# Kernel tuning notes

Hardware: AMD Instinct MI355X
Metric: run time of the kernel (lower is better)

## Reference

```python
import jax, jax.numpy as jnp
import numpy as np

N_HEAD, D_HEAD, D_MODEL = 8, 64, 512
QLEN, MLEN, BSZ = 1024, 1024, 4
KLEN = QLEN + MLEN
SCALE = 1.0 / (D_HEAD ** 0.5)
LN_EPS = 1e-5


def _rel_shift(x):
    # x: [qlen, rlen, bsz, n_head]
    q, rl, b, n = x.shape
    zero_pad = jnp.zeros((q, 1, b, n), x.dtype)
    x_padded = jnp.concatenate([zero_pad, x], axis=1).reshape(rl + 1, q, b, n)
    return x_padded[1:].reshape(q, rl, b, n)


def _layer_norm(x, g, b):
    mu = jnp.mean(x, axis=-1, keepdims=True)
    var = jnp.var(x, axis=-1, keepdims=True)
    return (x - mu) * jax.lax.rsqrt(var + LN_EPS) * g + b


def setup_inputs() -> dict:
    key = jax.random.key(0)
    ks = jax.random.split(key, 10)
    s = 0.02
    return {
        "w": jax.random.normal(ks[0], (QLEN, BSZ, D_MODEL), jnp.float32),
        "r": jax.random.normal(ks[1], (KLEN, 1, D_MODEL), jnp.float32),
        "r_w_bias": jax.random.normal(ks[2], (N_HEAD, D_HEAD), jnp.float32) * s,
        "r_r_bias": jax.random.normal(ks[3], (N_HEAD, D_HEAD), jnp.float32) * s,
        "mems": jax.random.normal(ks[4], (MLEN, BSZ, D_MODEL), jnp.float32),
        "Wq": jax.random.normal(ks[5], (D_MODEL, N_HEAD * D_HEAD), jnp.float32) * s,
        "Wkv": jax.random.normal(ks[6], (D_MODEL, 2 * N_HEAD * D_HEAD), jnp.float32) * s,
        "Wr": jax.random.normal(ks[7], (D_MODEL, N_HEAD * D_HEAD), jnp.float32) * s,
        "Wo": jax.random.normal(ks[8], (N_HEAD * D_HEAD, D_MODEL), jnp.float32) * s,
        "ln_g": jnp.ones((D_MODEL,), jnp.float32),
        "ln_b": jnp.zeros((D_MODEL,), jnp.float32),
        # causal mask: query i can attend keys j <= i + MLEN
        "attn_mask": jnp.arange(KLEN)[None, :] > (jnp.arange(QLEN) + MLEN)[:, None],
    }


def reference(w, r, r_w_bias, r_r_bias, mems, Wq, Wkv, Wr, Wo, ln_g, ln_b, attn_mask):
    qlen, bsz = w.shape[0], w.shape[1]
    cat = jnp.concatenate([mems, w], axis=0)          # [klen, bsz, d_model]
    klen = cat.shape[0]

    r_head_k = (r[:, 0] @ Wr).reshape(-1, N_HEAD, D_HEAD)   # [rlen, n, d]
    kv = cat @ Wkv                                           # [klen, bsz, 2*n*d]
    w_head_k, w_head_v = jnp.split(kv, 2, axis=-1)
    w_head_q = (cat[-qlen:] @ Wq).reshape(qlen, bsz, N_HEAD, D_HEAD)
    w_head_k = w_head_k.reshape(klen, bsz, N_HEAD, D_HEAD)
    w_head_v = w_head_v.reshape(klen, bsz, N_HEAD, D_HEAD)

    AC = jnp.einsum('ibnd,jbnd->ijbn', w_head_q + r_w_bias, w_head_k)
    BD = jnp.einsum('ibnd,jnd->ijbn', w_head_q + r_r_bias, r_head_k)
    BD = _rel_shift(BD)[:, :klen]

    attn_score = (AC + BD) * SCALE                           # [qlen, klen, bsz, n]
    attn_score = jnp.where(attn_mask[:, :, None, None], -jnp.inf, attn_score)
    attn_prob = jax.nn.softmax(attn_score, axis=1)

    attn_vec = jnp.einsum('ijbn,jbnd->ibnd', attn_prob, w_head_v)
    attn_vec = attn_vec.reshape(qlen, bsz, N_HEAD * D_HEAD)
    attn_out = attn_vec @ Wo
    return _layer_norm(w + attn_out, ln_g, ln_b)
```

## Files before the change

### kernel.cpp

```cpp
#include <hip/hip_runtime.h>
#include <hip/hip_bf16.h>
#include <math.h>

#define QLEN 1024
#define MLEN 1024
#define KLEN 2048
#define BSZ 4
#define NH 8
#define DH 64
#define DM 512
#define SCALE 0.125f
#define LN_EPS 1e-5f

#define RK_ROWS 2112

typedef __attribute__((ext_vector_type(8))) short short8;
typedef __attribute__((ext_vector_type(4))) float float4_;

#define GLB(p) ((const __attribute__((address_space(1))) void*)(p))
#define LDSP(p) ((__attribute__((address_space(3))) void*)(p))

__device__ inline ushort to_bf16(float x) {
  __hip_bfloat16 h = __float2bfloat16(x);
  return *reinterpret_cast<ushort*>(&h);
}
__device__ inline float bf16_to_f(ushort u) {
  union { unsigned int i; float f; } v;
  v.i = (unsigned int)u << 16;
  return v.f;
}

__device__ inline float row_max16(float v) {
  int x = __builtin_bit_cast(int, v);
  v = fmaxf(v, __builtin_bit_cast(float, __builtin_amdgcn_update_dpp(x, x, 0xB1, 0xF, 0xF, false)));
  x = __builtin_bit_cast(int, v);
  v = fmaxf(v, __builtin_bit_cast(float, __builtin_amdgcn_update_dpp(x, x, 0x4E, 0xF, 0xF, false)));
  x = __builtin_bit_cast(int, v);
  v = fmaxf(v, __builtin_bit_cast(float, __builtin_amdgcn_update_dpp(x, x, 0x124, 0xF, 0xF, false)));
  x = __builtin_bit_cast(int, v);
  v = fmaxf(v, __builtin_bit_cast(float, __builtin_amdgcn_update_dpp(x, x, 0x128, 0xF, 0xF, false)));
  return v;
}
__device__ inline float row_sum16(float v) {
  int x = __builtin_bit_cast(int, v);
  v += __builtin_bit_cast(float, __builtin_amdgcn_update_dpp(x, x, 0xB1, 0xF, 0xF, false));
  x = __builtin_bit_cast(int, v);
  v += __builtin_bit_cast(float, __builtin_amdgcn_update_dpp(x, x, 0x4E, 0xF, 0xF, false));
  x = __builtin_bit_cast(int, v);
  v += __builtin_bit_cast(float, __builtin_amdgcn_update_dpp(x, x, 0x124, 0xF, 0xF, false));
  x = __builtin_bit_cast(int, v);
  v += __builtin_bit_cast(float, __builtin_amdgcn_update_dpp(x, x, 0x128, 0xF, 0xF, false));
  return v;
}

__global__ __launch_bounds__(256) void wtrans_all(
    const float* __restrict__ Wq, const float* __restrict__ Wkv,
    const float* __restrict__ Wr, const float* __restrict__ Wo,
    ushort* __restrict__ WqT, ushort* __restrict__ WkvT,
    ushort* __restrict__ WrT, ushort* __restrict__ WoT) {
  __shared__ ushort tile[32][33];
  const int z = blockIdx.z;
  const float* W;
  ushort* WT;
  int N;
  if (z == 0)      { W = Wq;  WT = WqT;  N = DM; }
  else if (z == 1) { W = Wkv; WT = WkvT; N = 2 * DM; }
  else if (z == 2) { W = Wr;  WT = WrT;  N = DM; }
  else             { W = Wo;  WT = WoT;  N = DM; }
  const int k0 = blockIdx.x * 32, n0 = blockIdx.y * 32;
  if (n0 >= N) return;
  const int tid = threadIdx.x;
#pragma unroll
  for (int it = 0; it < 4; ++it) {
    int idx = tid + it * 256;
    int r = idx >> 5, c = idx & 31;
    tile[r][c] = to_bf16(W[(size_t)(k0 + r) * N + n0 + c]);
  }
  __syncthreads();
#pragma unroll
  for (int it = 0; it < 4; ++it) {
    int idx = tid + it * 256;
    int r = idx >> 5, c = idx & 31;
    WT[(size_t)(n0 + r) * DM + k0 + c] = tile[c][r];
  }
}

__global__ __launch_bounds__(256) void proj_all(
    const float* __restrict__ w, const float* __restrict__ mems,
    const float* __restrict__ r,
    const ushort* __restrict__ WqT, const ushort* __restrict__ WkvT,
    const ushort* __restrict__ WrT,
    const float* __restrict__ bias0, const float* __restrict__ bias1,
    ushort* __restrict__ qw, ushort* __restrict__ qr,
    ushort* __restrict__ k2, ushort* __restrict__ v2,
    ushort* __restrict__ rk2) {
  __shared__ ushort As[128 * 32];
  __shared__ ushort Bs[128 * 32];
  const int tid = threadIdx.x;
  int mode, bx, by;
  {
    int id = blockIdx.x;
    if (id < 128)      { mode = 0; bx = id >> 2;         by = id & 3; }
    else if (id < 640) { mode = 1; bx = (id - 128) >> 3; by = (id - 128) & 7; }
    else               { mode = 2; bx = (id - 640) >> 2; by = (id - 640) & 3; }
  }
  const int m0 = bx * 128, n0 = by * 128;
  const int wv = tid >> 6, lane = tid & 63;
  const int wm = wv >> 1, wn = wv & 1;
  const int l16 = lane & 15, quad = lane >> 4;

  const int arow = tid >> 1;
  const int acol = (tid & 1) * 16;
  const float* asrc;
  {
    int m = m0 + arow;
    if (mode == 2) asrc = r + (size_t)m * DM;
    else asrc = (m < QLEN * BSZ) ? w + (size_t)m * DM
                                 : mems + (size_t)(m - QLEN * BSZ) * DM;
    asrc += acol;
  }
  const ushort* BT = (mode == 0) ? WqT : (mode == 1) ? WkvT : WrT;
  const ushort* bsrc = BT + (size_t)(n0 + arow) * DM + acol;

  float4_ acc[4][4];
#pragma unroll
  for (int a = 0; a < 4; ++a)
#pragma unroll
    for (int b = 0; b < 4; ++b) acc[a][b] = float4_{0.f, 0.f, 0.f, 0.f};

  for (int k0 = 0; k0 < DM; k0 += 32) {
    float4 a0 = *reinterpret_cast<const float4*>(asrc + k0);
    float4 a1 = *reinterpret_cast<const float4*>(asrc + k0 + 4);
    float4 a2 = *reinterpret_cast<const float4*>(asrc + k0 + 8);
    float4 a3 = *reinterpret_cast<const float4*>(asrc + k0 + 12);
    ushort4 u0, u1, u2, u3;
    u0.x = to_bf16(a0.x); u0.y = to_bf16(a0.y); u0.z = to_bf16(a0.z); u0.w = to_bf16(a0.w);
    u1.x = to_bf16(a1.x); u1.y = to_bf16(a1.y); u1.z = to_bf16(a1.z); u1.w = to_bf16(a1.w);
    u2.x = to_bf16(a2.x); u2.y = to_bf16(a2.y); u2.z = to_bf16(a2.z); u2.w = to_bf16(a2.w);
    u3.x = to_bf16(a3.x); u3.y = to_bf16(a3.y); u3.z = to_bf16(a3.z); u3.w = to_bf16(a3.w);
    *reinterpret_cast<ushort4*>(&As[arow * 32 + acol]) = u0;
    *reinterpret_cast<ushort4*>(&As[arow * 32 + acol + 4]) = u1;
    *reinterpret_cast<ushort4*>(&As[arow * 32 + acol + 8]) = u2;
    *reinterpret_cast<ushort4*>(&As[arow * 32 + acol + 12]) = u3;
    *reinterpret_cast<uint4*>(&Bs[arow * 32 + acol]) =
        *reinterpret_cast<const uint4*>(bsrc + k0);
    *reinterpret_cast<uint4*>(&Bs[arow * 32 + acol + 8]) =
        *reinterpret_cast<const uint4*>(bsrc + k0 + 8);
    __syncthreads();
    short8 af[4], bf[4];
#pragma unroll
    for (int f = 0; f < 4; ++f) {
      af[f] = *reinterpret_cast<const short8*>(&As[(wm * 64 + f * 16 + l16) * 32 + quad * 8]);
      bf[f] = *reinterpret_cast<const short8*>(&Bs[(wn * 64 + f * 16 + l16) * 32 + quad * 8]);
    }
#pragma unroll
    for (int fm = 0; fm < 4; ++fm)
#pragma unroll
      for (int fn = 0; fn < 4; ++fn)
        acc[fm][fn] = __builtin_amdgcn_mfma_f32_16x16x32_bf16(bf[fn], af[fm], acc[fm][fn], 0, 0, 0);
    __syncthreads();
  }

#pragma unroll
  for (int fm = 0; fm < 4; ++fm) {
#pragma unroll
    for (int fn = 0; fn < 4; ++fn) {
      const int mm = m0 + wm * 64 + fm * 16 + l16;
      const int nnb = n0 + wn * 64 + fn * 16 + quad * 4;
      const float4_ a = acc[fm][fn];
      if (mode == 0) {
        float4 b0v = *reinterpret_cast<const float4*>(bias0 + nnb);
        float4 b1v = *reinterpret_cast<const float4*>(bias1 + nnb);
        int i = mm >> 2, b = mm & 3;
        int hd = nnb >> 6, d0 = nnb & 63;
        size_t idx = (((size_t)(b * NH + hd)) * QLEN + i) * DH + d0;
        ushort4 o0, o1;
        o0.x = to_bf16(a[0] + b0v.x); o0.y = to_bf16(a[1] + b0v.y);
        o0.z = to_bf16(a[2] + b0v.z); o0.w = to_bf16(a[3] + b0v.w);
        o1.x = to_bf16(a[0] + b1v.x); o1.y = to_bf16(a[1] + b1v.y);
        o1.z = to_bf16(a[2] + b1v.z); o1.w = to_bf16(a[3] + b1v.w);
        *reinterpret_cast<ushort4*>(qw + idx) = o0;
        *reinterpret_cast<ushort4*>(qr + idx) = o1;
      } else if (mode == 1) {
        int pos = mm >> 2, b = mm & 3;
        int jb = pos >> 5, jj = pos & 31;
        if (nnb < DM) {
          int hd = nnb >> 6, d = nnb & 63;
          int bn = b * NH + hd;
          int tile = ((jj >> 4) << 1) | (d >> 5);
          int lane2 = (((d >> 3) & 3) << 4) | (jj & 15);
          ushort4 o;
          o.x = to_bf16(a[0]); o.y = to_bf16(a[1]);
          o.z = to_bf16(a[2]); o.w = to_bf16(a[3]);
          *reinterpret_cast<ushort4*>(
              k2 + ((((size_t)bn * 64 + jb) * 4 + tile) * 64 + lane2) * 8 + (d & 7)) = o;
        } else {
          int nn2 = nnb - DM;
          int hd = nn2 >> 6, d = nn2 & 63;
          int bn = b * NH + hd;
          int tile = d >> 4;
          size_t base = ((((size_t)bn * 64 + jb) * 4 + tile) * 64 +
                         ((jj >> 3) << 4)) * 8 + (jj & 7);
#pragma unroll
          for (int reg = 0; reg < 4; ++reg)
            v2[base + (size_t)((d & 15) + reg) * 8] = to_bf16(a[reg]);
        }
      } else {
        int t = mm;
        int hd = nnb >> 6, d = nnb & 63;
        ushort4 o;
        o.x = to_bf16(a[0]); o.y = to_bf16(a[1]);
        o.z = to_bf16(a[2]); o.w = to_bf16(a[3]);
        *reinterpret_cast<ushort4*>(
            rk2 + ((size_t)hd * RK_ROWS + t) * DH + d) = o;
      }
    }
  }
}

__global__ __launch_bounds__(256) void mfma_out(
    const ushort* __restrict__ A, const ushort* __restrict__ BT,
    float* __restrict__ Y) {
  __shared__ ushort As[128 * 32];
  __shared__ ushort Bs[128 * 32];
  const int tid = threadIdx.x;
  const int m0 = blockIdx.x * 128, n0 = blockIdx.y * 128;
  const int wv = tid >> 6, lane = tid & 63;
  const int wm = wv >> 1, wn = wv & 1;
  const int l16 = lane & 15, quad = lane >> 4;
  const int arow = tid >> 1;
  const int acol = (tid & 1) * 16;
  const ushort* asrc = A + (size_t)(m0 + arow) * DM + acol;
  const ushort* bsrc = BT + (size_t)(n0 + arow) * DM + acol;

  float4_ acc[4][4];
#pragma unroll
  for (int a = 0; a < 4; ++a)
#pragma unroll
    for (int b = 0; b < 4; ++b) acc[a][b] = float4_{0.f, 0.f, 0.f, 0.f};

  for (int k0 = 0; k0 < DM; k0 += 32) {
    *reinterpret_cast<uint4*>(&As[arow * 32 + acol]) = *reinterpret_cast<const uint4*>(asrc + k0);
    *reinterpret_cast<uint4*>(&As[arow * 32 + acol + 8]) = *reinterpret_cast<const uint4*>(asrc + k0 + 8);
    *reinterpret_cast<uint4*>(&Bs[arow * 32 + acol]) = *reinterpret_cast<const uint4*>(bsrc + k0);
    *reinterpret_cast<uint4*>(&Bs[arow * 32 + acol + 8]) = *reinterpret_cast<const uint4*>(bsrc + k0 + 8);
    __syncthreads();
    short8 af[4], bf[4];
#pragma unroll
    for (int f = 0; f < 4; ++f) {
      af[f] = *reinterpret_cast<const short8*>(&As[(wm * 64 + f * 16 + l16) * 32 + quad * 8]);
      bf[f] = *reinterpret_cast<const short8*>(&Bs[(wn * 64 + f * 16 + l16) * 32 + quad * 8]);
    }
#pragma unroll
    for (int fm = 0; fm < 4; ++fm)
#pragma unroll
      for (int fn = 0; fn < 4; ++fn)
        acc[fm][fn] = __builtin_amdgcn_mfma_f32_16x16x32_bf16(bf[fn], af[fm], acc[fm][fn], 0, 0, 0);
    __syncthreads();
  }
#pragma unroll
  for (int fm = 0; fm < 4; ++fm)
#pragma unroll
    for (int fn = 0; fn < 4; ++fn) {
      int mm = m0 + wm * 64 + fm * 16 + l16;
      int nnb = n0 + wn * 64 + fn * 16 + quad * 4;
      float4 o;
      o.x = acc[fm][fn][0]; o.y = acc[fm][fn][1];
      o.z = acc[fm][fn][2]; o.w = acc[fm][fn][3];
      *reinterpret_cast<float4*>(Y + (size_t)mm * DM + nnb) = o;
    }
}

__global__ __launch_bounds__(256) void ln_fuse(
    const float* __restrict__ y, const float* __restrict__ wres,
    const float* __restrict__ g, const float* __restrict__ bb,
    float* __restrict__ out) {
  const int row = blockIdx.x * 4 + (threadIdx.x >> 6);
  const int lane = threadIdx.x & 63;
  const float* yr = y + (size_t)row * DM + lane * 4;
  const float* wr = wres + (size_t)row * DM + lane * 4;
  float4 x0 = *(const float4*)yr;
  float4 x1 = *(const float4*)(yr + 256);
  float4 w0 = *(const float4*)wr;
  float4 w1 = *(const float4*)(wr + 256);
  x0.x += w0.x; x0.y += w0.y; x0.z += w0.z; x0.w += w0.w;
  x1.x += w1.x; x1.y += w1.y; x1.z += w1.z; x1.w += w1.w;
  float s = x0.x + x0.y + x0.z + x0.w + x1.x + x1.y + x1.z + x1.w;
  float ss = x0.x * x0.x + x0.y * x0.y + x0.z * x0.z + x0.w * x0.w +
             x1.x * x1.x + x1.y * x1.y + x1.z * x1.z + x1.w * x1.w;
#pragma unroll
  for (int off = 1; off <= 32; off <<= 1) {
    s += __shfl_xor(s, off, 64);
    ss += __shfl_xor(ss, off, 64);
  }
  float mu = s * (1.f / DM);
  float var = ss * (1.f / DM) - mu * mu;
  float rstd = rsqrtf(var + LN_EPS);
  float4 g0 = *(const float4*)(g + lane * 4);
  float4 g1 = *(const float4*)(g + lane * 4 + 256);
  float4 b0 = *(const float4*)(bb + lane * 4);
  float4 b1 = *(const float4*)(bb + lane * 4 + 256);
  float4 o0, o1;
  o0.x = (x0.x - mu) * rstd * g0.x + b0.x;
  o0.y = (x0.y - mu) * rstd * g0.y + b0.y;
  o0.z = (x0.z - mu) * rstd * g0.z + b0.z;
  o0.w = (x0.w - mu) * rstd * g0.w + b0.w;
  o1.x = (x1.x - mu) * rstd * g1.x + b1.x;
  o1.y = (x1.y - mu) * rstd * g1.y + b1.y;
  o1.z = (x1.z - mu) * rstd * g1.z + b1.z;
  o1.w = (x1.w - mu) * rstd * g1.w + b1.w;
  float* orow = out + (size_t)row * DM + lane * 4;
  *reinterpret_cast<float4*>(orow) = o0;
  *reinterpret_cast<float4*>(orow + 256) = o1;
}

__global__ __launch_bounds__(256, 4) void attn_mfma(
    const ushort* __restrict__ qw, const ushort* __restrict__ qr,
    const ushort* __restrict__ k2, const ushort* __restrict__ v2,
    const ushort* __restrict__ rk2, ushort* __restrict__ Opart,
    float* __restrict__ ml) {
  const int i0b = (gridDim.x - 1 - blockIdx.x) * 64;
  const int n = blockIdx.y;
  const int b = blockIdx.z >> 1, seg = blockIdx.z & 1;
  const int bn = b * NH + n;
  const int tid = threadIdx.x;
  const int wv = tid >> 6, lane = tid & 63;
  const int l16 = lane & 15, quad = lane >> 4;
  const int i0w = i0b + wv * 16;

  __shared__ ushort stage[2][8 * 512];
  __shared__ float Dlds[4][16 * 66];
  __shared__ ushort Plds[4][16 * 32];
  float* __restrict__ Dw = Dlds[wv];
  ushort* __restrict__ Pw = Plds[wv];

  const ushort* __restrict__ k2b = k2 + (size_t)bn * (64 * 4 * 512);
  const ushort* __restrict__ v2b = v2 + (size_t)bn * (64 * 4 * 512);
  const ushort* __restrict__ rk2n = rk2 + (size_t)n * RK_ROWS * DH;

  const int nIterTot = (i0b + 63 + MLEN) / 32 + 1;
  const int nHalf = nIterTot >> 1;
  const int c0 = seg ? nHalf : 0;
  const int c1 = seg ? nIterTot : nHalf;

  short8 aqw0, aqw1, aqr0, aqr1;
  {
    const ushort* qwp = qw + (((size_t)bn * QLEN) + i0w + l16) * DH + quad * 8;
    const ushort* qrp = qr + (((size_t)bn * QLEN) + i0w + l16) * DH + quad * 8;
    aqw0 = *(const short8*)(qwp);
    aqw1 = *(const short8*)(qwp + 32);
    aqr0 = *(const short8*)(qrp);
    aqr1 = *(const short8*)(qrp + 32);
  }

  auto issue_dma = [&](int jb, int buf) {
#pragma unroll
    for (int s = 0; s < 2; ++s) {
      const int m = wv + s * 4;
      const ushort* base = (m < 4) ? k2b : v2b;
      const ushort* g = base + ((size_t)jb * 4 + (m & 3)) * 512 + lane * 8;
      __builtin_amdgcn_global_load_lds(GLB(g), LDSP(&stage[buf][m * 512]), 16, 0, 0);
    }
  };

  float4_ O[4];
#pragma unroll
  for (int t = 0; t < 4; ++t) O[t] = float4_{0.f, 0.f, 0.f, 0.f};
  float mrow[4] = {-INFINITY, -INFINITY, -INFINITY, -INFINITY};
  float lpart[4] = {0.f, 0.f, 0.f, 0.f};
  const float SL2E = SCALE * 1.44269504088896f;
  const int rbase = 48 - 16 * wv;

  issue_dma(c0, 0);
  issue_dma(c0 + 1, 1);

  for (int k = c0; k < c1; ++k) {
    __builtin_amdgcn_s_waitcnt(0x0F72);
    __builtin_amdgcn_sched_barrier(0);
    __builtin_amdgcn_s_barrier();
    __builtin_amdgcn_sched_barrier(0);
    const ushort* sb = stage[k & 1];
    const int j0 = k * 32;

    const int tbase = j0 - i0b + 960;
    short8 rb0[3], rb1[3];
#pragma unroll
    for (int tt = 0; tt < 3; ++tt) {
      const ushort* rrow = rk2n + (size_t)(tbase + rbase + tt * 16 + l16) * DH;
      rb0[tt] = *(const short8*)(rrow + quad * 8);
      rb1[tt] = *(const short8*)(rrow + (4 + quad) * 8);
    }

    float4_ ac[2];
#pragma unroll
    for (int h = 0; h < 2; ++h) {
      short8 b0 = *(const short8*)(sb + (h * 2 + 0) * 512 + lane * 8);
      short8 b1 = *(const short8*)(sb + (h * 2 + 1) * 512 + lane * 8);
      float4_ c = {0.f, 0.f, 0.f, 0.f};
      c = __builtin_amdgcn_mfma_f32_16x16x32_bf16(aqw0, b0, c, 0, 0, 0);
      c = __builtin_amdgcn_mfma_f32_16x16x32_bf16(aqw1, b1, c, 0, 0, 0);
      ac[h] = c;
    }
#pragma unroll
    for (int tt = 0; tt < 3; ++tt) {
      float4_ d = {0.f, 0.f, 0.f, 0.f};
      d = __builtin_amdgcn_mfma_f32_16x16x32_bf16(aqr0, rb0[tt], d, 0, 0, 0);
      d = __builtin_amdgcn_mfma_f32_16x16x32_bf16(aqr1, rb1[tt], d, 0, 0, 0);
#pragma unroll
      for (int rg = 0; rg < 4; ++rg) {
        int row = quad * 4 + rg;
        Dw[row * 66 + tt * 16 + l16 + row] = d[rg];
      }
    }
    float s[2][4];
#pragma unroll
    for (int half = 0; half < 2; ++half) {
#pragma unroll
      for (int rg = 0; rg < 4; ++rg) {
        int row = quad * 4 + rg;
        int jloc = half * 16 + l16;
        float bd = Dw[row * 66 + jloc + 15];
        float sv = (ac[half][rg] + bd) * SL2E;
        s[half][rg] = (j0 + jloc > i0w + row + MLEN) ? -INFINITY : sv;
      }
    }
#pragma unroll
    for (int rg = 0; rg < 4; ++rg) {
      float mx = row_max16(fmaxf(s[0][rg], s[1][rg]));
      float mn = fmaxf(mrow[rg], mx);
      float alpha = __builtin_amdgcn_exp2f(mrow[rg] - mn);
      float p0 = __builtin_amdgcn_exp2f(s[0][rg] - mn);
      float p1 = __builtin_amdgcn_exp2f(s[1][rg] - mn);
      lpart[rg] = lpart[rg] * alpha + (p0 + p1);
      mrow[rg] = mn;
#pragma unroll
      for (int t = 0; t < 4; ++t) O[t][rg] *= alpha;
      int row = quad * 4 + rg;
      int idx0 = (l16 >> 3) * 128 + row * 8 + (l16 & 7);
      Pw[idx0] = to_bf16(p0);
      Pw[idx0 + 256] = to_bf16(p1);
    }
    short8 pfrag = *(const short8*)(Pw + lane * 8);
#pragma unroll
    for (int t = 0; t < 4; ++t) {
      short8 vfrag = *(const short8*)(sb + (4 + t) * 512 + lane * 8);
      O[t] = __builtin_amdgcn_mfma_f32_16x16x32_bf16(pfrag, vfrag, O[t], 0, 0, 0);
    }

    __builtin_amdgcn_sched_barrier(0);
    __builtin_amdgcn_s_barrier();
    __builtin_amdgcn_sched_barrier(0);
    int jn = k + 2;
    if (jn > c1 - 1) jn = c1 - 1;
    issue_dma(jn, k & 1);
  }

  float lsum[4];
#pragma unroll
  for (int rg = 0; rg < 4; ++rg) lsum[rg] = row_sum16(lpart[rg]);
  ushort* op = Opart + (size_t)seg * QLEN * BSZ * DM;
  float2* mlp = (float2*)ml;
#pragma unroll
  for (int rg = 0; rg < 4; ++rg) {
    int row = quad * 4 + rg;
    if (l16 == 0) {
      mlp[((size_t)seg * QLEN * BSZ + (size_t)(i0w + row) * BSZ + b) * NH + n] =
          float2{mrow[rg], lsum[rg]};
    }
#pragma unroll
    for (int t = 0; t < 4; ++t) {
      op[((size_t)(i0w + row) * BSZ + b) * DM + n * DH + t * 16 + l16] =
          to_bf16(O[t][rg]);
    }
  }
}

__global__ __launch_bounds__(256) void attn_combine(
    const ushort* __restrict__ Opart, const float* __restrict__ ml,
    ushort* __restrict__ avbf) {
  const int row = blockIdx.x;
  const int tid = threadIdx.x;
  const int col = tid * 2;
  const int h = col >> 6;
  const float2* mlp = (const float2*)ml;
  float2 a = mlp[(size_t)row * NH + h];
  float2 c = mlp[((size_t)QLEN * BSZ + row) * NH + h];
  float M = fmaxf(a.x, c.x);
  float e0 = __builtin_amdgcn_exp2f(a.x - M);
  float e1 = __builtin_amdgcn_exp2f(c.x - M);
  float inv = 1.f / (a.y * e0 + c.y * e1);
  float s0 = e0 * inv, s1 = e1 * inv;
  size_t base = (size_t)row * DM + col;
  ushort2 o0 = *(const ushort2*)(Opart + base);
  ushort2 o1 = *(const ushort2*)(Opart + (size_t)QLEN * BSZ * DM + base);
  ushort2 o;
  o.x = to_bf16(bf16_to_f(o0.x) * s0 + bf16_to_f(o1.x) * s1);
  o.y = to_bf16(bf16_to_f(o0.y) * s0 + bf16_to_f(o1.y) * s1);
  *(ushort2*)(avbf + base) = o;
}

extern "C" void kernel_launch(void* const* d_in, const int* in_sizes, int n_in,
                              void* d_out, int out_size, void* d_ws, size_t ws_size,
                              hipStream_t stream) {
  const float* w    = (const float*)d_in[0];
  const float* r    = (const float*)d_in[1];
  const float* rwb  = (const float*)d_in[2];
  const float* rrb  = (const float*)d_in[3];
  const float* mems = (const float*)d_in[4];
  const float* Wq   = (const float*)d_in[5];
  const float* Wkv  = (const float*)d_in[6];
  const float* Wr   = (const float*)d_in[7];
  const float* Wo   = (const float*)d_in[8];
  const float* ln_g = (const float*)d_in[9];
  const float* ln_b = (const float*)d_in[10];
  float* out = (float*)d_out;

  char* p = (char*)d_ws;
  auto alloc = [&](size_t bytes) {
    char* q = p;
    p += (bytes + 255) & ~(size_t)255;
    return q;
  };
  ushort* WqT   = (ushort*)alloc((size_t)DM * DM * 2);
  ushort* WkvT  = (ushort*)alloc((size_t)2 * DM * DM * 2);
  ushort* WrT   = (ushort*)alloc((size_t)DM * DM * 2);
  ushort* WoT   = (ushort*)alloc((size_t)DM * DM * 2);
  ushort* qw    = (ushort*)alloc((size_t)BSZ * NH * QLEN * DH * 2);
  ushort* qr    = (ushort*)alloc((size_t)BSZ * NH * QLEN * DH * 2);
  ushort* k2    = (ushort*)alloc((size_t)BSZ * NH * 64 * 4 * 512 * 2);
  ushort* v2    = (ushort*)alloc((size_t)BSZ * NH * 64 * 4 * 512 * 2);
  ushort* rk2   = (ushort*)alloc((size_t)NH * RK_ROWS * DH * 2);
  ushort* avbf  = (ushort*)alloc((size_t)QLEN * BSZ * DM * 2);
  ushort* Opart = (ushort*)alloc((size_t)2 * QLEN * BSZ * DM * 2);
  float*  ml    = (float*)alloc((size_t)2 * QLEN * BSZ * NH * 2 * 4);
  float* y = (float*)k2;

  wtrans_all<<<dim3(16, 32, 4), dim3(256), 0, stream>>>(
      Wq, Wkv, Wr, Wo, WqT, WkvT, WrT, WoT);
  proj_all<<<dim3(704), dim3(256), 0, stream>>>(
      w, mems, r, WqT, WkvT, WrT, rwb, rrb, qw, qr, k2, v2, rk2);
  attn_mfma<<<dim3(QLEN / 64, NH, BSZ * 2), dim3(256), 0, stream>>>(
      qw, qr, k2, v2, rk2, Opart, ml);
  attn_combine<<<dim3(QLEN * BSZ), dim3(256), 0, stream>>>(Opart, ml, avbf);
  mfma_out<<<dim3(32, 4), dim3(256), 0, stream>>>(avbf, WoT, y);
  ln_fuse<<<dim3(QLEN * BSZ / 4), dim3(256), 0, stream>>>(y, w, ln_g, ln_b, out);
}
```

Measured before the change: 260.6 us.

## Widen attention key tile to 64, prefetch rel-pos keys, fuse split combine into out-proj

```diff
diff --git a/kernel.cpp b/kernel.cpp
--- a/kernel.cpp
+++ b/kernel.cpp
@@ -13,6 +13,7 @@
 #define LN_EPS 1e-5f
 
 #define RK_ROWS 2112
+#define DSTR 95
 
 typedef __attribute__((ext_vector_type(8))) short short8;
 typedef __attribute__((ext_vector_type(4))) float float4_;
@@ -218,8 +219,19 @@
   }
 }
 
+__device__ inline uint4 combine8(uint4 u0, uint4 u1, float s0, float s1) {
+  union U { uint4 v; ushort u[8]; };
+  U a, b, o;
+  a.v = u0; b.v = u1;
+#pragma unroll
+  for (int e = 0; e < 8; ++e)
+    o.u[e] = to_bf16(bf16_to_f(a.u[e]) * s0 + bf16_to_f(b.u[e]) * s1);
+  return o.v;
+}
+
 __global__ __launch_bounds__(256) void mfma_out(
-    const ushort* __restrict__ A, const ushort* __restrict__ BT,
+    const ushort* __restrict__ O0, const ushort* __restrict__ O1,
+    const float* __restrict__ ml, const ushort* __restrict__ BT,
     float* __restrict__ Y) {
   __shared__ ushort As[128 * 32];
   __shared__ ushort Bs[128 * 32];
@@ -230,8 +242,9 @@
   const int l16 = lane & 15, quad = lane >> 4;
   const int arow = tid >> 1;
   const int acol = (tid & 1) * 16;
-  const ushort* asrc = A + (size_t)(m0 + arow) * DM + acol;
+  const int row = m0 + arow;
   const ushort* bsrc = BT + (size_t)(n0 + arow) * DM + acol;
+  const float2* mlp = (const float2*)ml;
 
   float4_ acc[4][4];
 #pragma unroll
@@ -240,8 +253,22 @@
     for (int b = 0; b < 4; ++b) acc[a][b] = float4_{0.f, 0.f, 0.f, 0.f};
 
   for (int k0 = 0; k0 < DM; k0 += 32) {
-    *reinterpret_cast<uint4*>(&As[arow * 32 + acol]) = *reinterpret_cast<const uint4*>(asrc + k0);
-    *reinterpret_cast<uint4*>(&As[arow * 32 + acol + 8]) = *reinterpret_cast<const uint4*>(asrc + k0 + 8);
+    const int col0 = k0 + acol;
+    const int h = col0 >> 6;
+    float2 a = mlp[(size_t)row * NH + h];
+    float2 c = mlp[(size_t)(QLEN * BSZ + row) * NH + h];
+    float M = fmaxf(a.x, c.x);
+    float e0 = __builtin_amdgcn_exp2f(a.x - M);
+    float e1 = __builtin_amdgcn_exp2f(c.x - M);
+    float inv = 1.f / (a.y * e0 + c.y * e1);
+    float s0 = e0 * inv, s1 = e1 * inv;
+    size_t ob = (size_t)row * DM + col0;
+    uint4 u0a = *reinterpret_cast<const uint4*>(O0 + ob);
+    uint4 u0b = *reinterpret_cast<const uint4*>(O0 + ob + 8);
+    uint4 u1a = *reinterpret_cast<const uint4*>(O1 + ob);
+    uint4 u1b = *reinterpret_cast<const uint4*>(O1 + ob + 8);
+    *reinterpret_cast<uint4*>(&As[arow * 32 + acol]) = combine8(u0a, u1a, s0, s1);
+    *reinterpret_cast<uint4*>(&As[arow * 32 + acol + 8]) = combine8(u0b, u1b, s0, s1);
     *reinterpret_cast<uint4*>(&Bs[arow * 32 + acol]) = *reinterpret_cast<const uint4*>(bsrc + k0);
     *reinterpret_cast<uint4*>(&Bs[arow * 32 + acol + 8]) = *reinterpret_cast<const uint4*>(bsrc + k0 + 8);
     __syncthreads();
@@ -314,7 +341,7 @@
   *reinterpret_cast<float4*>(orow + 256) = o1;
 }
 
-__global__ __launch_bounds__(256, 4) void attn_mfma(
+__global__ __launch_bounds__(256, 2) void attn_mfma(
     const ushort* __restrict__ qw, const ushort* __restrict__ qr,
     const ushort* __restrict__ k2, const ushort* __restrict__ v2,
     const ushort* __restrict__ rk2, ushort* __restrict__ Opart,
@@ -328,9 +355,9 @@
   const int l16 = lane & 15, quad = lane >> 4;
   const int i0w = i0b + wv * 16;
 
-  __shared__ ushort stage[2][8 * 512];
-  __shared__ float Dlds[4][16 * 66];
-  __shared__ ushort Plds[4][16 * 32];
+  __shared__ ushort stage[2][16 * 512];
+  __shared__ float Dlds[4][16 * DSTR];
+  __shared__ ushort Plds[4][1024];
   float* __restrict__ Dw = Dlds[wv];
   ushort* __restrict__ Pw = Plds[wv];
 
@@ -338,7 +365,7 @@
   const ushort* __restrict__ v2b = v2 + (size_t)bn * (64 * 4 * 512);
   const ushort* __restrict__ rk2n = rk2 + (size_t)n * RK_ROWS * DH;
 
-  const int nIterTot = (i0b + 63 + MLEN) / 32 + 1;
+  const int nIterTot = i0b / 64 + 17;
   const int nHalf = nIterTot >> 1;
   const int c0 = seg ? nHalf : 0;
   const int c1 = seg ? nIterTot : nHalf;
@@ -355,10 +382,12 @@
 
   auto issue_dma = [&](int jb, int buf) {
 #pragma unroll
-    for (int s = 0; s < 2; ++s) {
+    for (int s = 0; s < 4; ++s) {
       const int m = wv + s * 4;
-      const ushort* base = (m < 4) ? k2b : v2b;
-      const ushort* g = base + ((size_t)jb * 4 + (m & 3)) * 512 + lane * 8;
+      const int mk = m & 7;
+      const ushort* base = (m < 8) ? k2b : v2b;
+      const ushort* g = base +
+          ((size_t)(jb * 2 + (mk >> 2)) * 4 + (mk & 3)) * 512 + lane * 8;
       __builtin_amdgcn_global_load_lds(GLB(g), LDSP(&stage[buf][m * 512]), 16, 0, 0);
     }
   };
@@ -369,90 +398,117 @@
   float mrow[4] = {-INFINITY, -INFINITY, -INFINITY, -INFINITY};
   float lpart[4] = {0.f, 0.f, 0.f, 0.f};
   const float SL2E = SCALE * 1.44269504088896f;
-  const int rbase = 48 - 16 * wv;
+
+  short8 rbA0[5], rbA1[5], rbN0[5], rbN1[5];
 
   issue_dma(c0, 0);
+  {
+    const int tb0 = c0 * 64 - i0b + 1008 - 16 * wv + l16;
+#pragma unroll
+    for (int tt = 0; tt < 5; ++tt) {
+      const ushort* rrow = rk2n + (size_t)(tb0 + tt * 16) * DH;
+      rbA0[tt] = *(const short8*)(rrow + quad * 8);
+      rbA1[tt] = *(const short8*)(rrow + (4 + quad) * 8);
+    }
+  }
   issue_dma(c0 + 1, 1);
 
   for (int k = c0; k < c1; ++k) {
-    __builtin_amdgcn_s_waitcnt(0x0F72);
+    __builtin_amdgcn_s_waitcnt(0x0F74);
     __builtin_amdgcn_sched_barrier(0);
     __builtin_amdgcn_s_barrier();
     __builtin_amdgcn_sched_barrier(0);
-    const ushort* sb = stage[k & 1];
-    const int j0 = k * 32;
-
-    const int tbase = j0 - i0b + 960;
-    short8 rb0[3], rb1[3];
-#pragma unroll
-    for (int tt = 0; tt < 3; ++tt) {
-      const ushort* rrow = rk2n + (size_t)(tbase + rbase + tt * 16 + l16) * DH;
-      rb0[tt] = *(const short8*)(rrow + quad * 8);
-      rb1[tt] = *(const short8*)(rrow + (4 + quad) * 8);
-    }
-
-    float4_ ac[2];
-#pragma unroll
-    for (int h = 0; h < 2; ++h) {
-      short8 b0 = *(const short8*)(sb + (h * 2 + 0) * 512 + lane * 8);
-      short8 b1 = *(const short8*)(sb + (h * 2 + 1) * 512 + lane * 8);
+    const ushort* sb = stage[(k - c0) & 1];
+    const int j0 = k * 64;
+
+    __builtin_amdgcn_s_setprio(1);
+    float4_ ac[4];
+#pragma unroll
+    for (int h = 0; h < 4; ++h) {
+      const ushort* kb = sb + (((h >> 1) * 4 + (h & 1) * 2) * 512) + lane * 8;
+      short8 b0 = *(const short8*)(kb);
+      short8 b1 = *(const short8*)(kb + 512);
       float4_ c = {0.f, 0.f, 0.f, 0.f};
       c = __builtin_amdgcn_mfma_f32_16x16x32_bf16(aqw0, b0, c, 0, 0, 0);
       c = __builtin_amdgcn_mfma_f32_16x16x32_bf16(aqw1, b1, c, 0, 0, 0);
       ac[h] = c;
     }
 #pragma unroll
-    for (int tt = 0; tt < 3; ++tt) {
+    for (int tt = 0; tt < 5; ++tt) {
       float4_ d = {0.f, 0.f, 0.f, 0.f};
-      d = __builtin_amdgcn_mfma_f32_16x16x32_bf16(aqr0, rb0[tt], d, 0, 0, 0);
-      d = __builtin_amdgcn_mfma_f32_16x16x32_bf16(aqr1, rb1[tt], d, 0, 0, 0);
+      d = __builtin_amdgcn_mfma_f32_16x16x32_bf16(aqr0, rbA0[tt], d, 0, 0, 0);
+      d = __builtin_amdgcn_mfma_f32_16x16x32_bf16(aqr1, rbA1[tt], d, 0, 0, 0);
 #pragma unroll
       for (int rg = 0; rg < 4; ++rg) {
         int row = quad * 4 + rg;
-        Dw[row * 66 + tt * 16 + l16 + row] = d[rg];
+        Dw[row * DSTR + tt * 16 + l16 + row] = d[rg];
       }
     }
-    float s[2][4];
-#pragma unroll
-    for (int half = 0; half < 2; ++half) {
+    __builtin_amdgcn_s_setprio(0);
+
+    {
+      int kn = k + 1; if (kn > c1 - 1) kn = c1 - 1;
+      const int tbN = kn * 64 - i0b + 1008 - 16 * wv + l16;
+#pragma unroll
+      for (int tt = 0; tt < 5; ++tt) {
+        const ushort* rrow = rk2n + (size_t)(tbN + tt * 16) * DH;
+        rbN0[tt] = *(const short8*)(rrow + quad * 8);
+        rbN1[tt] = *(const short8*)(rrow + (4 + quad) * 8);
+      }
+    }
+
+    float s4[4][4];
+#pragma unroll
+    for (int hh = 0; hh < 4; ++hh)
 #pragma unroll
       for (int rg = 0; rg < 4; ++rg) {
         int row = quad * 4 + rg;
-        int jloc = half * 16 + l16;
-        float bd = Dw[row * 66 + jloc + 15];
-        float sv = (ac[half][rg] + bd) * SL2E;
-        s[half][rg] = (j0 + jloc > i0w + row + MLEN) ? -INFINITY : sv;
+        int jloc = hh * 16 + l16;
+        float bd = Dw[row * DSTR + jloc + 15];
+        float sv = (ac[hh][rg] + bd) * SL2E;
+        s4[hh][rg] = (j0 + jloc > i0w + row + MLEN) ? -INFINITY : sv;
       }
-    }
 #pragma unroll
     for (int rg = 0; rg < 4; ++rg) {
-      float mx = row_max16(fmaxf(s[0][rg], s[1][rg]));
+      float mx = row_max16(fmaxf(fmaxf(s4[0][rg], s4[1][rg]),
+                                 fmaxf(s4[2][rg], s4[3][rg])));
       float mn = fmaxf(mrow[rg], mx);
       float alpha = __builtin_amdgcn_exp2f(mrow[rg] - mn);
-      float p0 = __builtin_amdgcn_exp2f(s[0][rg] - mn);
-      float p1 = __builtin_amdgcn_exp2f(s[1][rg] - mn);
-      lpart[rg] = lpart[rg] * alpha + (p0 + p1);
+      float p0 = __builtin_amdgcn_exp2f(s4[0][rg] - mn);
+      float p1 = __builtin_amdgcn_exp2f(s4[1][rg] - mn);
+      float p2 = __builtin_amdgcn_exp2f(s4[2][rg] - mn);
+      float p3 = __builtin_amdgcn_exp2f(s4[3][rg] - mn);
+      lpart[rg] = lpart[rg] * alpha + (p0 + p1 + p2 + p3);
       mrow[rg] = mn;
 #pragma unroll
       for (int t = 0; t < 4; ++t) O[t][rg] *= alpha;
       int row = quad * 4 + rg;
-      int idx0 = (l16 >> 3) * 128 + row * 8 + (l16 & 7);
-      Pw[idx0] = to_bf16(p0);
-      Pw[idx0 + 256] = to_bf16(p1);
-    }
-    short8 pfrag = *(const short8*)(Pw + lane * 8);
+      int pbase = (l16 >> 3) * 128 + row * 8 + (l16 & 7);
+      Pw[pbase]       = to_bf16(p0);
+      Pw[pbase + 256] = to_bf16(p1);
+      Pw[pbase + 512] = to_bf16(p2);
+      Pw[pbase + 768] = to_bf16(p3);
+    }
+    short8 pf0 = *(const short8*)(Pw + lane * 8);
+    short8 pf1 = *(const short8*)(Pw + 512 + lane * 8);
+    __builtin_amdgcn_s_setprio(1);
 #pragma unroll
     for (int t = 0; t < 4; ++t) {
-      short8 vfrag = *(const short8*)(sb + (4 + t) * 512 + lane * 8);
-      O[t] = __builtin_amdgcn_mfma_f32_16x16x32_bf16(pfrag, vfrag, O[t], 0, 0, 0);
-    }
+      short8 vf0 = *(const short8*)(sb + (8 + t) * 512 + lane * 8);
+      short8 vf1 = *(const short8*)(sb + (12 + t) * 512 + lane * 8);
+      O[t] = __builtin_amdgcn_mfma_f32_16x16x32_bf16(pf0, vf0, O[t], 0, 0, 0);
+      O[t] = __builtin_amdgcn_mfma_f32_16x16x32_bf16(pf1, vf1, O[t], 0, 0, 0);
+    }
+    __builtin_amdgcn_s_setprio(0);
 
     __builtin_amdgcn_sched_barrier(0);
     __builtin_amdgcn_s_barrier();
     __builtin_amdgcn_sched_barrier(0);
     int jn = k + 2;
     if (jn > c1 - 1) jn = c1 - 1;
-    issue_dma(jn, k & 1);
+    issue_dma(jn, (k - c0) & 1);
+#pragma unroll
+    for (int tt = 0; tt < 5; ++tt) { rbA0[tt] = rbN0[tt]; rbA1[tt] = rbN1[tt]; }
   }
 
   float lsum[4];
@@ -473,30 +529,6 @@
           to_bf16(O[t][rg]);
     }
   }
-}
-
-__global__ __launch_bounds__(256) void attn_combine(
-    const ushort* __restrict__ Opart, const float* __restrict__ ml,
-    ushort* __restrict__ avbf) {
-  const int row = blockIdx.x;
-  const int tid = threadIdx.x;
-  const int col = tid * 2;
-  const int h = col >> 6;
-  const float2* mlp = (const float2*)ml;
-  float2 a = mlp[(size_t)row * NH + h];
-  float2 c = mlp[((size_t)QLEN * BSZ + row) * NH + h];
-  float M = fmaxf(a.x, c.x);
-  float e0 = __builtin_amdgcn_exp2f(a.x - M);
-  float e1 = __builtin_amdgcn_exp2f(c.x - M);
-  float inv = 1.f / (a.y * e0 + c.y * e1);
-  float s0 = e0 * inv, s1 = e1 * inv;
-  size_t base = (size_t)row * DM + col;
-  ushort2 o0 = *(const ushort2*)(Opart + base);
-  ushort2 o1 = *(const ushort2*)(Opart + (size_t)QLEN * BSZ * DM + base);
-  ushort2 o;
-  o.x = to_bf16(bf16_to_f(o0.x) * s0 + bf16_to_f(o1.x) * s1);
-  o.y = to_bf16(bf16_to_f(o0.y) * s0 + bf16_to_f(o1.y) * s1);
-  *(ushort2*)(avbf + base) = o;
 }
 
 extern "C" void kernel_launch(void* const* d_in, const int* in_sizes, int n_in,
@@ -530,7 +562,6 @@
   ushort* k2    = (ushort*)alloc((size_t)BSZ * NH * 64 * 4 * 512 * 2);
   ushort* v2    = (ushort*)alloc((size_t)BSZ * NH * 64 * 4 * 512 * 2);
   ushort* rk2   = (ushort*)alloc((size_t)NH * RK_ROWS * DH * 2);
-  ushort* avbf  = (ushort*)alloc((size_t)QLEN * BSZ * DM * 2);
   ushort* Opart = (ushort*)alloc((size_t)2 * QLEN * BSZ * DM * 2);
   float*  ml    = (float*)alloc((size_t)2 * QLEN * BSZ * NH * 2 * 4);
   float* y = (float*)k2;
@@ -541,7 +572,7 @@
       w, mems, r, WqT, WkvT, WrT, rwb, rrb, qw, qr, k2, v2, rk2);
   attn_mfma<<<dim3(QLEN / 64, NH, BSZ * 2), dim3(256), 0, stream>>>(
       qw, qr, k2, v2, rk2, Opart, ml);
-  attn_combine<<<dim3(QLEN * BSZ), dim3(256), 0, stream>>>(Opart, ml, avbf);
-  mfma_out<<<dim3(32, 4), dim3(256), 0, stream>>>(avbf, WoT, y);
+  mfma_out<<<dim3(32, 4), dim3(256), 0, stream>>>(
+      Opart, Opart + (size_t)QLEN * BSZ * DM, ml, WoT, y);
   ln_fuse<<<dim3(QLEN * BSZ / 4), dim3(256), 0, stream>>>(y, w, ln_g, ln_b, out);
 }
```

Measured after the change: 262.3 us. About the same (+0.6%).
